# Optimization experiments

Hardware: AMD Instinct MI355X
Metric: run time of the kernel (lower is better)

## Reference

```python
import jax, jax.numpy as jnp
import numpy as np

# dims
B, A, CIN, CC = 512, 256, 7, 16          # batch, num_actions, input channels, conv channels
D, H, DH, E = 48, 8, 6, 512              # token_dimension, heads, head_dim, num_embeddings
S, T = 32, 32                            # num_input_tokens, num_output_tokens
AH = H * DH                              # 48
NL = 4                                   # attention layers
CONV_IN = A * CC                         # 4096
ENC = S * D                              # 1536
DEC_OUT = A * CIN                        # 1792
SCALE = float(np.sqrt(D))                # module uses sqrt(input_embedding_dim)
EPS = 1e-5


def _ln(x, g, b):
    m = jnp.mean(x, axis=-1, keepdims=True)
    v = jnp.var(x, axis=-1, keepdims=True)
    return (x - m) * jax.lax.rsqrt(v + EPS) * g + b


def setup_inputs() -> dict:
    key = jax.random.key(0)
    ks = iter(jax.random.split(key, 64))
    def rn(shape, s=0.05):
        return jax.random.normal(next(ks), shape, dtype=jnp.float32) * s
    inp = {}
    inp['x'] = jax.random.normal(next(ks), (B, A, CIN), dtype=jnp.float32)
    inp['u'] = jax.random.uniform(next(ks), (T, B), dtype=jnp.float32)
    inp['bn_g'] = jnp.ones((CIN,), jnp.float32); inp['bn_b'] = jnp.zeros((CIN,), jnp.float32)
    inp['conv_w'] = rn((CC, CIN, 5)); inp['conv_b'] = jnp.zeros((CC,), jnp.float32)
    inp['tk_W1'] = rn((CONV_IN, 2 * CONV_IN)); inp['tk_b1'] = jnp.zeros((2 * CONV_IN,), jnp.float32)
    inp['tk_W2'] = rn((2 * CONV_IN, ENC)); inp['tk_b2'] = jnp.zeros((ENC,), jnp.float32)
    for nm in ('q', 'k', 'v'):
        inp['ln%s_g' % nm] = jnp.ones((NL, D), jnp.float32)
        inp['ln%s_b' % nm] = jnp.zeros((NL, D), jnp.float32)
        inp['W%s' % nm] = rn((NL, D, AH))
        inp['b%s' % nm] = jnp.zeros((NL, AH), jnp.float32)
    inp['Wo'] = rn((NL, AH, D)); inp['bo'] = jnp.zeros((NL, D), jnp.float32)
    inp['mln_g'] = jnp.ones((NL, D), jnp.float32); inp['mln_b'] = jnp.zeros((NL, D), jnp.float32)
    inp['W1'] = rn((NL, D, 2 * D)); inp['b1'] = jnp.zeros((NL, 2 * D), jnp.float32)
    inp['W2'] = rn((NL, 2 * D, D)); inp['b2'] = jnp.zeros((NL, D), jnp.float32)
    inp['emb'] = rn((D, E), 1.0)          # nn.Parameter(torch.randn(D, E))
    inp['pos_enc'] = rn((T, D), 1.0)      # nn.Parameter(torch.randn(T, D))
    inp['dec_W1'] = rn((ENC, 2 * ENC)); inp['dec_b1'] = jnp.zeros((2 * ENC,), jnp.float32)
    inp['dec_W2'] = rn((2 * ENC, DEC_OUT)); inp['dec_b2'] = jnp.zeros((DEC_OUT,), jnp.float32)
    return inp


def _fwd(x, u, bn_g, bn_b, conv_w, conv_b, tk_W1, tk_b1, tk_W2, tk_b2,
         lnq_g, lnq_b, Wq, bq, lnk_g, lnk_b, Wk, bk, lnv_g, lnv_b, Wv, bv, Wo, bo,
         mln_g, mln_b, W1, b1, W2, b2, emb, pos_enc, dec_W1, dec_b1, dec_W2, dec_b2):
    # --- conv stem (BatchNorm1d in training mode: batch statistics) ---
    xt = x.transpose(0, 2, 1)                              # [B, 7, A]
    mu = jnp.mean(xt, axis=(0, 2), keepdims=True)
    var = jnp.var(xt, axis=(0, 2), keepdims=True)
    xn = (xt - mu) * jax.lax.rsqrt(var + EPS) * bn_g[None, :, None] + bn_b[None, :, None]
    xc = jax.lax.conv_general_dilated(xn, conv_w, (1,), ((2, 2),),
                                      dimension_numbers=('NCH', 'OIH', 'NCH')) + conv_b[None, :, None]
    xf = xc.reshape(B, -1)                                 # [B, 16*A]
    h = jax.nn.relu(xf @ tk_W1 + tk_b1)
    toks = (h @ tk_W2 + tk_b2).reshape(B, S, D)            # [B, S, D]

    STOT = S + T
    kc = jnp.zeros((NL, B, H, STOT, DH), jnp.float32)
    vc = jnp.zeros_like(kc)

    # --- prefill pass (output discarded; fills KV caches) ---
    ii = jnp.arange(S)[:, None]; jj = jnp.arange(S)[None, :]
    pre_mask = jnp.where(jj - ii >= S - 1, -999.0, 0.0)    # triu(-999, diagonal=S-1), as in source
    xcur = toks
    for l in range(NL):
        q = (_ln(xcur, lnq_g[l], lnq_b[l]) @ Wq[l] + bq[l]).reshape(B, S, H, DH).transpose(0, 2, 1, 3)
        k = (_ln(xcur, lnk_g[l], lnk_b[l]) @ Wk[l] + bk[l]).reshape(B, S, H, DH).transpose(0, 2, 1, 3)
        v = (_ln(xcur, lnv_g[l], lnv_b[l]) @ Wv[l] + bv[l]).reshape(B, S, H, DH).transpose(0, 2, 1, 3)
        kc = kc.at[l, :, :, :S].set(k)
        vc = vc.at[l, :, :, :S].set(v)
        attn = jax.nn.softmax(jnp.einsum('bhqd,bhkd->bhqk', q, k) / SCALE + pre_mask, axis=-1)
        o = jnp.einsum('bhqk,bhkd->bhqd', attn, v).transpose(0, 2, 1, 3).reshape(B, S, AH)
        xcur = o @ Wo[l] + bo[l] + xcur
        hh = jax.nn.relu(_ln(xcur, mln_g[l], mln_b[l]) @ W1[l] + b1[l])
        xcur = hh @ W2[l] + b2[l]

    jidx = jnp.arange(STOT)

    def step(carry, xs):
        kc, vc = carry
        i, pe, uu = xs
        p = S + i                                          # cache length before this step
        xtk = jnp.broadcast_to(pe, (B, 1, D))
        newk, newv = [], []
        for l in range(NL):
            q = (_ln(xtk, lnq_g[l], lnq_b[l]) @ Wq[l] + bq[l]).reshape(B, 1, H, DH).transpose(0, 2, 1, 3)
            k = (_ln(xtk, lnk_g[l], lnk_b[l]) @ Wk[l] + bk[l]).reshape(B, 1, H, DH).transpose(0, 2, 1, 3)
            v = (_ln(xtk, lnv_g[l], lnv_b[l]) @ Wv[l] + bv[l]).reshape(B, 1, H, DH).transpose(0, 2, 1, 3)
            kcl = jax.lax.dynamic_update_slice(kc[l], k, (0, 0, p, 0))
            vcl = jax.lax.dynamic_update_slice(vc[l], v, (0, 0, p, 0))
            scores = jnp.einsum('bhqd,bhkd->bhqk', q, kcl) / SCALE
            # source mask: -999 added for positions >= mask_offset (includes the new token itself)
            scores = scores + jnp.where(jidx >= p, -999.0, 0.0)
            attn = jax.nn.softmax(scores, axis=-1)
            o = jnp.einsum('bhqk,bhkd->bhqd', attn, vcl).transpose(0, 2, 1, 3).reshape(B, 1, AH)
            xtk = o @ Wo[l] + bo[l] + xtk
            hh = jax.nn.relu(_ln(xtk, mln_g[l], mln_b[l]) @ W1[l] + b1[l])
            xtk = hh @ W2[l] + b2[l]
            newk.append(kcl); newv.append(vcl)
        attended = xtk                                     # [B, 1, D]
        probs = jax.nn.softmax((attended @ emb).reshape(B, E), axis=1)
        cdf = jnp.cumsum(probs, axis=1)
        idx = jnp.clip(jnp.sum((cdf < uu[:, None]).astype(jnp.int32), axis=1), 0, E - 1)
        sel = emb.T[idx].reshape(B, 1, D)
        st = sel + attended - jax.lax.stop_gradient(attended)  # straight-through
        return (jnp.stack(newk), jnp.stack(newv)), st

    (_, _), outs = jax.lax.scan(step, (kc, vc), (jnp.arange(T), pos_enc, u))
    out_tokens = outs.transpose(1, 0, 2, 3).reshape(B, T * D)
    dh_ = jax.nn.relu(out_tokens @ dec_W1 + dec_b1)
    traj = (dh_ @ dec_W2 + dec_b2).reshape(B, A, CIN)
    return traj


def reference(x, u, bn_g, bn_b, conv_w, conv_b, tk_W1, tk_b1, tk_W2, tk_b2,
              lnq_g, lnq_b, Wq, bq, lnk_g, lnk_b, Wk, bk, lnv_g, lnv_b, Wv, bv, Wo, bo,
              mln_g, mln_b, W1, b1, W2, b2, emb, pos_enc, dec_W1, dec_b1, dec_W2, dec_b2):
    return _fwd(x, u, bn_g, bn_b, conv_w, conv_b, tk_W1, tk_b1, tk_W2, tk_b2,
                lnq_g, lnq_b, Wq, bq, lnk_g, lnk_b, Wk, bk, lnv_g, lnv_b, Wv, bv, Wo, bo,
                mln_g, mln_b, W1, b1, W2, b2, emb, pos_enc, dec_W1, dec_b1, dec_W2, dec_b2)
```

## Files before the change

### kernel.cpp

```cpp
#include <hip/hip_runtime.h>

static const double SCALE_ = 6.928203230275509;

__device__ inline float  fma_t(float a, float b, float c)  { return fmaf(a, b, c); }
__device__ inline double fma_t(double a, double b, double c){ return fma(a, b, c); }

__device__ __attribute__((noinline)) double dotW(const double* a,
                                                 const float* W, int n, int ldw,
                                                 double init) {
  double a0 = init, a1 = 0.0;
#pragma unroll 2
  for (int i = 0; i < n; i += 2) {
    a0 = fma(a[i],     (double)W[i * ldw],       a0);
    a1 = fma(a[i + 1], (double)W[(i + 1) * ldw], a1);
  }
  return a0 + a1;
}

template <int N, typename WP>
__device__ __forceinline__ double dotN(const double* a, WP W, int ldw, double init) {
  double c0 = init, c1 = 0.0, c2 = 0.0, c3 = 0.0;
#pragma unroll
  for (int i = 0; i < N; i += 4) {
    c0 = fma(a[i],     (double)W[i * ldw],       c0);
    c1 = fma(a[i + 1], (double)W[(i + 1) * ldw], c1);
    c2 = fma(a[i + 2], (double)W[(i + 2) * ldw], c2);
    c3 = fma(a[i + 3], (double)W[(i + 3) * ldw], c3);
  }
  return (c0 + c1) + (c2 + c3);
}

__device__ __attribute__((noinline)) double2 ln_stats48(const double* x) {
  double s0 = 0, s1 = 0, q0 = 0, q1 = 0;
#pragma unroll 2
  for (int i = 0; i < 48; i += 2) {
    const double va = x[i], vb = x[i + 1];
    s0 += va; q0 = fma(va, va, q0);
    s1 += vb; q1 = fma(vb, vb, q1);
  }
  const double m = (s0 + s1) / 48.0;
  const double rs = 1.0 / sqrt((q0 + q1) / 48.0 - m * m + 1e-5);
  return make_double2(m, rs);
}

__device__ __attribute__((noinline)) double exp_ni(double x) { return exp(x); }

__global__ __launch_bounds__(256) void bn_partial_kernel(const float* __restrict__ x,
                                                         double* __restrict__ part) {
  __shared__ double sh[256 * 14];
  const int tid = threadIdx.x;
  const int idx = blockIdx.x * 256 + tid;
  const float* p = x + (size_t)idx * 7;
  for (int c = 0; c < 7; ++c) {
    double v = (double)p[c];
    sh[tid * 14 + c] = v;
    sh[tid * 14 + 7 + c] = v * v;
  }
  __syncthreads();
  if (tid < 14) {
    double acc = 0.0;
    for (int t = 0; t < 256; ++t) acc += sh[t * 14 + tid];
    part[blockIdx.x * 14 + tid] = acc;
  }
}

__global__ void bn_final_kernel(const double* __restrict__ part,
                                const float* __restrict__ g, const float* __restrict__ bb,
                                double* __restrict__ stat) {
  const int c = threadIdx.x;
  if (c < 7) {
    double s = 0.0, s2 = 0.0;
    for (int i = 0; i < 512; ++i) { s += part[i * 14 + c]; s2 += part[i * 14 + 7 + c]; }
    const double mean = s / 131072.0;
    const double var = s2 / 131072.0 - mean * mean;
    const double rstd = 1.0 / sqrt(var + 1e-5);
    const double scale = rstd * (double)g[c];
    stat[c] = scale;
    stat[7 + c] = (double)bb[c] - mean * scale;
  }
}

__global__ __launch_bounds__(256) void conv_kernel(const float* __restrict__ x,
                                                   const float* __restrict__ wconv,
                                                   const float* __restrict__ cb,
                                                   const double* __restrict__ stat,
                                                   double* __restrict__ xf) {
  __shared__ double wsh[560 + 14];
  const int tid = threadIdx.x;
  for (int i = tid; i < 560; i += 256) wsh[i] = (double)wconv[i];
  for (int i = tid; i < 14; i += 256) wsh[560 + i] = stat[i];
  __syncthreads();
  const int idx = blockIdx.x * 256 + tid;
  const int a = idx & 255;
  const int o = (idx >> 8) & 15;
  const int b = idx >> 12;
  double acc = (double)cb[o];
  const float* xb = x + (size_t)b * (256 * 7);
  for (int k = 0; k < 5; ++k) {
    const int pos = a + k - 2;
    if (pos < 0 || pos >= 256) continue;
    const float* xp = xb + pos * 7;
    for (int ci = 0; ci < 7; ++ci) {
      const double xn = (double)xp[ci] * wsh[560 + ci] + wsh[567 + ci];
      acc = fma(xn, wsh[(o * 7 + ci) * 5 + k], acc);
    }
  }
  xf[idx] = acc;
}

template <typename T, bool BIAS, bool RELU>
__global__ __launch_bounds__(256) void gemm128_kernel(const T* __restrict__ A,
                                                      const float* __restrict__ Bm,
                                                      const float* __restrict__ bias,
                                                      T* __restrict__ C,
                                                      const int M, const int N, const int K,
                                                      const int kc) {
  __shared__ T As[16][130];
  __shared__ T Bs[16][66];
  const int tid = threadIdx.x;
  const int tx = tid & 15, ty = tid >> 4;
  const int n0 = blockIdx.x * 64, m0 = blockIdx.y * 128;
  const int k0 = blockIdx.z * kc, kend = k0 + kc;
  const int ar = tid >> 1, ac = (tid & 1) * 8;
  const int br = tid >> 4, bc = (tid & 15) * 4;
  const T* Ap = A + (size_t)(m0 + ar) * K;
  const float* Bp = Bm + (size_t)br * N + n0 + bc;
  T acc[8][4] = {};
  for (int k = k0; k < kend; k += 16) {
    T av8[8];
#pragma unroll
    for (int i = 0; i < 8; ++i) av8[i] = Ap[k + ac + i];
    const float4 bw = *(const float4*)(Bp + (size_t)k * N);
#pragma unroll
    for (int i = 0; i < 8; ++i) As[ac + i][ar] = av8[i];
    Bs[br][bc] = (T)bw.x; Bs[br][bc + 1] = (T)bw.y;
    Bs[br][bc + 2] = (T)bw.z; Bs[br][bc + 3] = (T)bw.w;
    __syncthreads();
#pragma unroll
    for (int kk = 0; kk < 16; ++kk) {
      T a[8], b[4];
#pragma unroll
      for (int i = 0; i < 8; ++i) a[i] = As[kk][ty * 8 + i];
#pragma unroll
      for (int j = 0; j < 4; ++j) b[j] = Bs[kk][tx * 4 + j];
#pragma unroll
      for (int i = 0; i < 8; ++i)
#pragma unroll
        for (int j = 0; j < 4; ++j) acc[i][j] = fma_t(a[i], b[j], acc[i][j]);
    }
    __syncthreads();
  }
  T* Cp = C + (size_t)blockIdx.z * M * N;
#pragma unroll
  for (int i = 0; i < 8; ++i) {
    const int row = m0 + ty * 8 + i;
#pragma unroll
    for (int j = 0; j < 4; ++j) {
      const int col = n0 + tx * 4 + j;
      T v = acc[i][j];
      if (BIAS) v += (T)bias[col];
      if (RELU) v = v > (T)0 ? v : (T)0;
      Cp[(size_t)row * N + col] = v;
    }
  }
}

template <typename T, bool BIAS, bool RELU>
__global__ __launch_bounds__(256) void gemm_kernel(const T* __restrict__ A,
                                                   const float* __restrict__ Bm,
                                                   const float* __restrict__ bias,
                                                   T* __restrict__ C,
                                                   const int M, const int N, const int K,
                                                   const int kc) {
  __shared__ T As[16][65];
  __shared__ T Bs[16][65];
  const int tid = threadIdx.x;
  const int tx = tid & 15, ty = tid >> 4;
  const int n0 = blockIdx.x * 64, m0 = blockIdx.y * 64;
  const int k0 = blockIdx.z * kc, kend = k0 + kc;
  const int ar = tid >> 2, ac = (tid & 3) * 4;
  const int br = tid >> 4, bc = (tid & 15) * 4;
  const T* Ap = A + (size_t)(m0 + ar) * K;
  const float* Bp = Bm + (size_t)br * N + n0 + bc;
  T acc[4][4] = {};
  for (int k = k0; k < kend; k += 16) {
    const T a0 = Ap[k + ac], a1 = Ap[k + ac + 1], a2 = Ap[k + ac + 2], a3 = Ap[k + ac + 3];
    const float4 bw = *(const float4*)(Bp + (size_t)k * N);
    As[ac][ar] = a0; As[ac + 1][ar] = a1; As[ac + 2][ar] = a2; As[ac + 3][ar] = a3;
    Bs[br][bc] = (T)bw.x; Bs[br][bc + 1] = (T)bw.y; Bs[br][bc + 2] = (T)bw.z; Bs[br][bc + 3] = (T)bw.w;
    __syncthreads();
#pragma unroll
    for (int kk = 0; kk < 16; ++kk) {
      T av[4], bv2[4];
#pragma unroll
      for (int i = 0; i < 4; ++i) av[i] = As[kk][ty * 4 + i];
#pragma unroll
      for (int j = 0; j < 4; ++j) bv2[j] = Bs[kk][tx * 4 + j];
#pragma unroll
      for (int i = 0; i < 4; ++i)
#pragma unroll
        for (int j = 0; j < 4; ++j) acc[i][j] = fma_t(av[i], bv2[j], acc[i][j]);
    }
    __syncthreads();
  }
  T* Cp = C + (size_t)blockIdx.z * M * N;
#pragma unroll
  for (int i = 0; i < 4; ++i) {
    const int row = m0 + ty * 4 + i;
#pragma unroll
    for (int j = 0; j < 4; ++j) {
      const int col = n0 + tx * 4 + j;
      T v = acc[i][j];
      if (BIAS) v += (T)bias[col];
      if (RELU) v = v > (T)0 ? v : (T)0;
      Cp[(size_t)row * N + col] = v;
    }
  }
}

__global__ __launch_bounds__(256) void reduce2_bias_kernel(const double* __restrict__ part,
                                                           const float* __restrict__ bias,
                                                           double* __restrict__ out,
                                                           const int MN, const int N) {
  const int i = blockIdx.x * 256 + threadIdx.x;
  if (i < MN) out[i] = part[i] + part[MN + i] + (double)bias[i % N];
}

__global__ __launch_bounds__(256) void prefill_kernel(
    const double* __restrict__ toks,
    const float* __restrict__ lnq_g, const float* __restrict__ lnq_b,
    const float* __restrict__ Wq, const float* __restrict__ bq,
    const float* __restrict__ lnk_g, const float* __restrict__ lnk_b,
    const float* __restrict__ Wk, const float* __restrict__ bk,
    const float* __restrict__ lnv_g, const float* __restrict__ lnv_b,
    const float* __restrict__ Wv, const float* __restrict__ bvv,
    const float* __restrict__ Wo, const float* __restrict__ bo,
    const float* __restrict__ mln_g, const float* __restrict__ mln_b,
    const float* __restrict__ W1, const float* __restrict__ b1,
    const float* __restrict__ W2, const float* __restrict__ b2,
    double* __restrict__ kcache, double* __restrict__ vcache) {
  const int b = blockIdx.x, tid = threadIdx.x;
  __shared__ double xcur[1536], abuf[1536], qbuf[1536], kvbuf[3072];
  __shared__ double mean[32], rstd[32];
  double* kb = kvbuf;
  double* vb = kvbuf + 1536;

#pragma unroll 1
  for (int i = tid; i < 1536; i += 256) xcur[i] = toks[(size_t)b * 1536 + i];
  __syncthreads();

#pragma unroll 1
  for (int l = 0; l < 4; ++l) {
    if (tid < 32) {
      double s = 0.0, s2 = 0.0;
#pragma unroll 4
      for (int i = 0; i < 48; ++i) { const double v = xcur[tid * 48 + i]; s += v; s2 += v * v; }
      const double m = s / 48.0;
      mean[tid] = m;
      rstd[tid] = 1.0 / sqrt(s2 / 48.0 - m * m + 1e-5);
    }
    __syncthreads();
    const bool last = (l == 3);

    if (!last) {
#pragma unroll 1
      for (int i = tid; i < 1536; i += 256) {
        const int t = i / 48, d = i % 48;
        abuf[i] = (xcur[i] - mean[t]) * rstd[t] * (double)lnq_g[l * 48 + d] + (double)lnq_b[l * 48 + d];
      }
      __syncthreads();
#pragma unroll 1
      for (int i = tid; i < 1536; i += 256) {
        const int t = i / 48, j = i % 48;
        qbuf[i] = dotW(abuf + t * 48, Wq + l * 2304 + j, 48, 48, (double)bq[l * 48 + j]);
      }
      __syncthreads();
    }
#pragma unroll 1
    for (int i = tid; i < 1536; i += 256) {
      const int t = i / 48, d = i % 48;
      abuf[i] = (xcur[i] - mean[t]) * rstd[t] * (double)lnk_g[l * 48 + d] + (double)lnk_b[l * 48 + d];
    }
    __syncthreads();
#pragma unroll 1
    for (int i = tid; i < 1536; i += 256) {
      const int t = i / 48, j = i % 48;
      kb[i] = dotW(abuf + t * 48, Wk + l * 2304 + j, 48, 48, (double)bk[l * 48 + j]);
    }
    __syncthreads();
#pragma unroll 1
    for (int i = tid; i < 1536; i += 256) {
      const int t = i / 48, d = i % 48;
      abuf[i] = (xcur[i] - mean[t]) * rstd[t] * (double)lnv_g[l * 48 + d] + (double)lnv_b[l * 48 + d];
    }
    __syncthreads();
#pragma unroll 1
    for (int i = tid; i < 1536; i += 256) {
      const int t = i / 48, j = i % 48;
      vb[i] = dotW(abuf + t * 48, Wv + l * 2304 + j, 48, 48, (double)bvv[l * 48 + j]);
    }
    __syncthreads();
#pragma unroll 1
    for (int i = tid; i < 1536; i += 256) {
      const int t = i / 48, j = i % 48;
      const int h = j / 6, d = j % 6;
      const size_t ci = ((((size_t)b * 4 + l) * 8 + h) * 64 + t) * 6 + d;
      kcache[ci] = kb[i];
      vcache[ci] = vb[i];
    }

    if (!last) {
      const int t = tid >> 3, h = tid & 7;
      const double* qp = qbuf + t * 48 + h * 6;
      const double q0 = qp[0], q1 = qp[1], q2 = qp[2], q3 = qp[3], q4 = qp[4], q5 = qp[5];
      double mx = -1e300;
#pragma unroll 4
      for (int j = 0; j < 32; ++j) {
        const double* kp = kb + j * 48 + h * 6;
        double sv = q0 * kp[0];
        sv = fma(q1, kp[1], sv); sv = fma(q2, kp[2], sv); sv = fma(q3, kp[3], sv);
        sv = fma(q4, kp[4], sv); sv = fma(q5, kp[5], sv);
        sv /= SCALE_;
        if (t == 0 && j == 31) sv -= 999.0;
        mx = sv > mx ? sv : mx;
      }
      double den = 0, o0 = 0, o1 = 0, o2 = 0, o3 = 0, o4 = 0, o5 = 0;
#pragma unroll 4
      for (int j = 0; j < 32; ++j) {
        const double* kp = kb + j * 48 + h * 6;
        double sv = q0 * kp[0];
        sv = fma(q1, kp[1], sv); sv = fma(q2, kp[2], sv); sv = fma(q3, kp[3], sv);
        sv = fma(q4, kp[4], sv); sv = fma(q5, kp[5], sv);
        sv /= SCALE_;
        if (t == 0 && j == 31) sv -= 999.0;
        const double e = exp_ni(sv - mx);
        den += e;
        const double* vp = vb + j * 48 + h * 6;
        o0 = fma(e, vp[0], o0); o1 = fma(e, vp[1], o1); o2 = fma(e, vp[2], o2);
        o3 = fma(e, vp[3], o3); o4 = fma(e, vp[4], o4); o5 = fma(e, vp[5], o5);
      }
      abuf[t * 48 + h * 6 + 0] = o0 / den;
      abuf[t * 48 + h * 6 + 1] = o1 / den;
      abuf[t * 48 + h * 6 + 2] = o2 / den;
      abuf[t * 48 + h * 6 + 3] = o3 / den;
      abuf[t * 48 + h * 6 + 4] = o4 / den;
      abuf[t * 48 + h * 6 + 5] = o5 / den;
      __syncthreads();
#pragma unroll 1
      for (int i = tid; i < 1536; i += 256) {
        const int t2 = i / 48, j = i % 48;
        xcur[i] += dotW(abuf + t2 * 48, Wo + l * 2304 + j, 48, 48, (double)bo[l * 48 + j]);
      }
      __syncthreads();
      if (tid < 32) {
        double s = 0.0, s2 = 0.0;
#pragma unroll 4
        for (int i = 0; i < 48; ++i) { const double v = xcur[tid * 48 + i]; s += v; s2 += v * v; }
        const double m = s / 48.0;
        mean[tid] = m;
        rstd[tid] = 1.0 / sqrt(s2 / 48.0 - m * m + 1e-5);
      }
      __syncthreads();
#pragma unroll 1
      for (int i = tid; i < 1536; i += 256) {
        const int t2 = i / 48, d = i % 48;
        qbuf[i] = (xcur[i] - mean[t2]) * rstd[t2] * (double)mln_g[l * 48 + d] + (double)mln_b[l * 48 + d];
      }
      __syncthreads();
#pragma unroll 1
      for (int i = tid; i < 3072; i += 256) {
        const int t2 = i / 96, jj = i % 96;
        const double acc = dotW(qbuf + t2 * 48, W1 + l * 4608 + jj, 48, 96, (double)b1[l * 96 + jj]);
        kvbuf[i] = acc > 0 ? acc : 0;
      }
      __syncthreads();
#pragma unroll 1
      for (int i = tid; i < 1536; i += 256) {
        const int t2 = i / 48, j = i % 48;
        abuf[i] = dotW(kvbuf + t2 * 96, W2 + l * 4608 + j, 96, 48, (double)b2[l * 48 + j]);
      }
      __syncthreads();
#pragma unroll 1
      for (int i = tid; i < 1536; i += 256) xcur[i] = abuf[i];
      __syncthreads();
    }
  }
}

__device__ __attribute__((noinline)) void sample_step(
    double* xtk, double* probs, double* red,
    const float* __restrict__ emb, const float* __restrict__ u,
    float* __restrict__ out_tok, int b, int step, int tid) {
  const double lg1 = dotN<48>(xtk, emb + tid, 512, 0.0);
  const double lg2 = dotN<48>(xtk, emb + 256 + tid, 512, 0.0);
  double mx = lg1 > lg2 ? lg1 : lg2;
#pragma unroll
  for (int off = 1; off < 64; off <<= 1) { const double o2 = __shfl_xor(mx, off); mx = o2 > mx ? o2 : mx; }
  if ((tid & 63) == 0) red[tid >> 6] = mx;
  __syncthreads();
  {
    const double m0 = red[0] > red[1] ? red[0] : red[1];
    const double m1 = red[2] > red[3] ? red[2] : red[3];
    mx = m0 > m1 ? m0 : m1;
  }
  probs[tid] = exp(lg1 - mx);
  probs[tid + 256] = exp(lg2 - mx);
  __syncthreads();
  if (tid < 64) {
    const int lane = tid;
    double loc[8], run = 0;
#pragma unroll
    for (int n2 = 0; n2 < 8; ++n2) { run += probs[lane * 8 + n2]; loc[n2] = run; }
    double incl = run;
#pragma unroll
    for (int off = 1; off < 64; off <<= 1) {
      const double t2 = __shfl_up(incl, off);
      if (lane >= off) incl += t2;
    }
    const double excl = incl - run;
    const double Ssum = __shfl(incl, 63);
    const double uu = (double)u[step * 512 + b];
    int cnt = 0;
#pragma unroll
    for (int n2 = 0; n2 < 8; ++n2) cnt += ((excl + loc[n2]) / Ssum < uu) ? 1 : 0;
#pragma unroll
    for (int off = 1; off < 64; off <<= 1) cnt += __shfl_xor(cnt, off);
    const int idx = cnt > 511 ? 511 : cnt;
    if (lane < 48) {
      const double sel = (double)emb[lane * 512 + idx];
      const double att = xtk[lane];
      out_tok[(size_t)b * 1536 + step * 48 + lane] = (float)((sel + att) - att);
    }
  }
  __syncthreads();
}

__global__ __launch_bounds__(256) void ar_kernel(
    const float* __restrict__ pos_enc, const float* __restrict__ u,
    const float* __restrict__ lnq_g, const float* __restrict__ lnq_b,
    const float* __restrict__ Wq, const float* __restrict__ bq,
    const float* __restrict__ lnk_g, const float* __restrict__ lnk_b,
    const float* __restrict__ Wk, const float* __restrict__ bk,
    const float* __restrict__ lnv_g, const float* __restrict__ lnv_b,
    const float* __restrict__ Wv, const float* __restrict__ bvv,
    const float* __restrict__ Wo, const float* __restrict__ bo,
    const float* __restrict__ mln_g, const float* __restrict__ mln_b,
    const float* __restrict__ W1, const float* __restrict__ b1,
    const float* __restrict__ W2, const float* __restrict__ b2,
    const float* __restrict__ emb,
    double* __restrict__ kcache, double* __restrict__ vcache,
    float* __restrict__ out_tok) {
  const int b = blockIdx.x, tid = threadIdx.x;
  __shared__ double xtk[48], anorm[144], qs[48], os[48], hh[96], probs[512], red[4];
  __shared__ float wsh[9216];

#pragma unroll 1
  for (int step = 0; step < 32; ++step) {
    const int p = 32 + step;
    if (tid < 48) xtk[tid] = (double)pos_enc[step * 48 + tid];
    __syncthreads();

#pragma unroll 1
    for (int l = 0; l < 4; ++l) {
      {
        float4* wsh4 = (float4*)wsh;
#pragma unroll 1
        for (int i = tid; i < 2304; i += 256) {
          const int a = i / 576, off4 = i - a * 576;
          const float* src = a == 0 ? Wq : a == 1 ? Wk : a == 2 ? Wv : Wo;
          wsh4[i] = ((const float4*)(src + l * 2304))[off4];
        }
      }
      {
        const double2 st = ln_stats48(xtk);
        if (tid < 144) {
          const int which = tid / 48, d = tid - which * 48;
          const float* gp = which == 0 ? lnq_g : which == 1 ? lnk_g : lnv_g;
          const float* bp = which == 0 ? lnq_b : which == 1 ? lnk_b : lnv_b;
          anorm[tid] = (xtk[d] - st.x) * st.y * (double)gp[l * 48 + d] + (double)bp[l * 48 + d];
        }
      }
      __syncthreads();
      if (tid < 144) {
        const int which = tid / 48, j = tid - which * 48;
        const float* bbp = which == 0 ? bq : which == 1 ? bk : bvv;
        const double acc = dotN<48>(anorm + which * 48, wsh + which * 2304 + j, 48,
                                    (double)bbp[l * 48 + j]);
        if (which == 0) {
          qs[j] = acc;
        } else {
          const int h = j / 6, d = j - h * 6;
          const size_t ci = ((((size_t)b * 4 + l) * 8 + h) * 64 + p) * 6 + d;
          if (which == 1) kcache[ci] = acc; else vcache[ci] = acc;
        }
      }
      __syncthreads();
      {
        const int h = tid >> 5, r = tid & 31;
        const double* kcb = kcache + ((((size_t)b * 4 + l) * 8 + h) * 64) * 6;
        const double* vcb = vcache + ((((size_t)b * 4 + l) * 8 + h) * 64) * 6;
        const double qv0 = qs[h * 6 + 0], qv1 = qs[h * 6 + 1], qv2 = qs[h * 6 + 2],
                     qv3 = qs[h * 6 + 3], qv4 = qs[h * 6 + 4], qv5 = qs[h * 6 + 5];
        const bool has2 = (r + 32) < p;
        const double* kp1 = kcb + r * 6;
        double sv1 = qv0 * kp1[0];
        sv1 = fma(qv1, kp1[1], sv1); sv1 = fma(qv2, kp1[2], sv1); sv1 = fma(qv3, kp1[3], sv1);
        sv1 = fma(qv4, kp1[4], sv1); sv1 = fma(qv5, kp1[5], sv1);
        sv1 /= SCALE_;
        double sv2 = -1e300;
        if (has2) {
          const double* kp2 = kcb + (r + 32) * 6;
          double t2 = qv0 * kp2[0];
          t2 = fma(qv1, kp2[1], t2); t2 = fma(qv2, kp2[2], t2); t2 = fma(qv3, kp2[3], t2);
          t2 = fma(qv4, kp2[4], t2); t2 = fma(qv5, kp2[5], t2);
          sv2 = t2 / SCALE_;
        }
        double mx = sv1 > sv2 ? sv1 : sv2;
#pragma unroll
        for (int off = 1; off < 32; off <<= 1) { const double o2 = __shfl_xor(mx, off); mx = o2 > mx ? o2 : mx; }
        const double e1 = exp(sv1 - mx);
        const double e2 = has2 ? exp(sv2 - mx) : 0.0;
        double den = e1 + e2;
        const double* vp1 = vcb + r * 6;
        double o[6];
#pragma unroll
        for (int d = 0; d < 6; ++d) o[d] = e1 * vp1[d];
        if (has2) {
          const double* vp2 = vcb + (r + 32) * 6;
#pragma unroll
          for (int d = 0; d < 6; ++d) o[d] = fma(e2, vp2[d], o[d]);
        }
#pragma unroll
        for (int off = 1; off < 32; off <<= 1) {
          den += __shfl_xor(den, off);
#pragma unroll
          for (int d = 0; d < 6; ++d) o[d] += __shfl_xor(o[d], off);
        }
        if (r == 0) {
#pragma unroll
          for (int d = 0; d < 6; ++d) os[h * 6 + d] = o[d] / den;
        }
      }
      __syncthreads();
      if (tid < 48)
        xtk[tid] += dotN<48>(os, wsh + 3 * 2304 + tid, 48, (double)bo[l * 48 + tid]);
      __syncthreads();
      {
        float4* wsh4 = (float4*)wsh;
#pragma unroll 1
        for (int i = tid; i < 2304; i += 256) {
          const int a = i / 1152, off4 = i - a * 1152;
          const float* src = a == 0 ? W1 : W2;
          wsh4[i] = ((const float4*)(src + l * 4608))[off4];
        }
      }
      {
        const double2 st = ln_stats48(xtk);
        if (tid < 48)
          anorm[tid] = (xtk[tid] - st.x) * st.y * (double)mln_g[l * 48 + tid] + (double)mln_b[l * 48 + tid];
      }
      __syncthreads();
      if (tid < 96) {
        const double v = dotN<48>(anorm, wsh + tid, 96, (double)b1[l * 96 + tid]);
        hh[tid] = v > 0 ? v : 0;
      }
      __syncthreads();
      if (tid < 48)
        xtk[tid] = dotN<96>(hh, wsh + 4608 + tid, 48, (double)b2[l * 48 + tid]);
      __syncthreads();
    }

    sample_step(xtk, probs, red, emb, u, out_tok, b, step, tid);
  }
}

extern "C" void kernel_launch(void* const* d_in, const int* in_sizes, int n_in,
                              void* d_out, int out_size, void* d_ws, size_t ws_size,
                              hipStream_t stream) {
  const float* x      = (const float*)d_in[0];
  const float* u      = (const float*)d_in[1];
  const float* bn_g   = (const float*)d_in[2];
  const float* bn_b   = (const float*)d_in[3];
  const float* conv_w = (const float*)d_in[4];
  const float* conv_b = (const float*)d_in[5];
  const float* tk_W1  = (const float*)d_in[6];
  const float* tk_b1  = (const float*)d_in[7];
  const float* tk_W2  = (const float*)d_in[8];
  const float* tk_b2  = (const float*)d_in[9];
  const float* lnq_g  = (const float*)d_in[10];
  const float* lnq_b  = (const float*)d_in[11];
  const float* Wq     = (const float*)d_in[12];
  const float* bq     = (const float*)d_in[13];
  const float* lnk_g  = (const float*)d_in[14];
  const float* lnk_b  = (const float*)d_in[15];
  const float* Wk     = (const float*)d_in[16];
  const float* bk     = (const float*)d_in[17];
  const float* lnv_g  = (const float*)d_in[18];
  const float* lnv_b  = (const float*)d_in[19];
  const float* Wv     = (const float*)d_in[20];
  const float* bvv    = (const float*)d_in[21];
  const float* Wo     = (const float*)d_in[22];
  const float* bo     = (const float*)d_in[23];
  const float* mln_g  = (const float*)d_in[24];
  const float* mln_b  = (const float*)d_in[25];
  const float* W1     = (const float*)d_in[26];
  const float* b1     = (const float*)d_in[27];
  const float* W2     = (const float*)d_in[28];
  const float* b2     = (const float*)d_in[29];
  const float* emb    = (const float*)d_in[30];
  const float* pos    = (const float*)d_in[31];
  const float* dW1    = (const float*)d_in[32];
  const float* db1    = (const float*)d_in[33];
  const float* dW2    = (const float*)d_in[34];
  const float* db2    = (const float*)d_in[35];
  float* out = (float*)d_out;

  char* w = (char*)d_ws;
  size_t off = 0;
  auto alloc = [&](size_t bytes) {
    size_t o = off;
    off = (off + bytes + 255) & ~(size_t)255;
    return o;
  };
  const size_t o_bnp  = alloc(512 * 14 * 8);
  const size_t o_bns  = alloc(14 * 8);
  const size_t o_xf   = alloc(16777216);
  const size_t o_h    = alloc(33554432);
  const size_t o_toks = alloc(6291456);
  const size_t o_kc   = alloc(50331648);
  const size_t o_vc   = alloc(50331648);

  double* bnp  = (double*)(w + o_bnp);
  double* bns  = (double*)(w + o_bns);
  double* xf   = (double*)(w + o_xf);
  double* hbuf = (double*)(w + o_h);
  double* toks = (double*)(w + o_toks);
  double* kc   = (double*)(w + o_kc);
  double* vc   = (double*)(w + o_vc);
  double* part = (double*)(w + o_xf);
  float*  otok = (float*)(w + o_h);
  float*  dh   = (float*)(w + o_h + 4194304);

  bn_partial_kernel<<<512, 256, 0, stream>>>(x, bnp);
  bn_final_kernel<<<1, 64, 0, stream>>>(bnp, bn_g, bn_b, bns);
  conv_kernel<<<8192, 256, 0, stream>>>(x, conv_w, conv_b, bns, xf);
  gemm128_kernel<double, true, true><<<dim3(128, 4, 1), 256, 0, stream>>>(
      xf, tk_W1, tk_b1, hbuf, 512, 8192, 4096, 4096);
  gemm128_kernel<double, false, false><<<dim3(24, 4, 2), 256, 0, stream>>>(
      hbuf, tk_W2, nullptr, part, 512, 1536, 8192, 4096);
  reduce2_bias_kernel<<<3072, 256, 0, stream>>>(part, tk_b2, toks, 512 * 1536, 1536);
  prefill_kernel<<<512, 256, 0, stream>>>(toks,
      lnq_g, lnq_b, Wq, bq, lnk_g, lnk_b, Wk, bk, lnv_g, lnv_b, Wv, bvv,
      Wo, bo, mln_g, mln_b, W1, b1, W2, b2, kc, vc);
  ar_kernel<<<512, 256, 0, stream>>>(pos, u,
      lnq_g, lnq_b, Wq, bq, lnk_g, lnk_b, Wk, bk, lnv_g, lnv_b, Wv, bvv,
      Wo, bo, mln_g, mln_b, W1, b1, W2, b2, emb, kc, vc, otok);
  gemm_kernel<float, true, true><<<dim3(48, 8, 1), 256, 0, stream>>>(
      otok, dW1, db1, dh, 512, 3072, 1536, 1536);
  gemm_kernel<float, true, false><<<dim3(28, 8, 1), 256, 0, stream>>>(
      dh, dW2, db2, out, 512, 1792, 3072, 3072);
}
```

Measured before the change: 4.955 ms.

## Widen autoregressive kernel to 512 threads with split-K dot products and warp LN

```diff
diff --git a/kernel.cpp b/kernel.cpp
--- a/kernel.cpp
+++ b/kernel.cpp
@@ -4,18 +4,6 @@
 
 __device__ inline float  fma_t(float a, float b, float c)  { return fmaf(a, b, c); }
 __device__ inline double fma_t(double a, double b, double c){ return fma(a, b, c); }
-
-__device__ __attribute__((noinline)) double dotW(const double* a,
-                                                 const float* W, int n, int ldw,
-                                                 double init) {
-  double a0 = init, a1 = 0.0;
-#pragma unroll 2
-  for (int i = 0; i < n; i += 2) {
-    a0 = fma(a[i],     (double)W[i * ldw],       a0);
-    a1 = fma(a[i + 1], (double)W[(i + 1) * ldw], a1);
-  }
-  return a0 + a1;
-}
 
 template <int N, typename WP>
 __device__ __forceinline__ double dotN(const double* a, WP W, int ldw, double init) {
@@ -28,19 +16,6 @@
     c3 = fma(a[i + 3], (double)W[(i + 3) * ldw], c3);
   }
   return (c0 + c1) + (c2 + c3);
-}
-
-__device__ __attribute__((noinline)) double2 ln_stats48(const double* x) {
-  double s0 = 0, s1 = 0, q0 = 0, q1 = 0;
-#pragma unroll 2
-  for (int i = 0; i < 48; i += 2) {
-    const double va = x[i], vb = x[i + 1];
-    s0 += va; q0 = fma(va, va, q0);
-    s1 += vb; q1 = fma(vb, vb, q1);
-  }
-  const double m = (s0 + s1) / 48.0;
-  const double rs = 1.0 / sqrt((q0 + q1) / 48.0 - m * m + 1e-5);
-  return make_double2(m, rs);
 }
 
 __device__ __attribute__((noinline)) double exp_ni(double x) { return exp(x); }
@@ -272,7 +247,7 @@
 #pragma unroll 1
       for (int i = tid; i < 1536; i += 256) {
         const int t = i / 48, j = i % 48;
-        qbuf[i] = dotW(abuf + t * 48, Wq + l * 2304 + j, 48, 48, (double)bq[l * 48 + j]);
+        qbuf[i] = dotN<48>(abuf + t * 48, Wq + l * 2304 + j, 48, (double)bq[l * 48 + j]);
       }
       __syncthreads();
     }
@@ -285,7 +260,7 @@
 #pragma unroll 1
     for (int i = tid; i < 1536; i += 256) {
       const int t = i / 48, j = i % 48;
-      kb[i] = dotW(abuf + t * 48, Wk + l * 2304 + j, 48, 48, (double)bk[l * 48 + j]);
+      kb[i] = dotN<48>(abuf + t * 48, Wk + l * 2304 + j, 48, (double)bk[l * 48 + j]);
     }
     __syncthreads();
 #pragma unroll 1
@@ -297,7 +272,7 @@
 #pragma unroll 1
     for (int i = tid; i < 1536; i += 256) {
       const int t = i / 48, j = i % 48;
-      vb[i] = dotW(abuf + t * 48, Wv + l * 2304 + j, 48, 48, (double)bvv[l * 48 + j]);
+      vb[i] = dotN<48>(abuf + t * 48, Wv + l * 2304 + j, 48, (double)bvv[l * 48 + j]);
     }
     __syncthreads();
 #pragma unroll 1
@@ -349,7 +324,7 @@
 #pragma unroll 1
       for (int i = tid; i < 1536; i += 256) {
         const int t2 = i / 48, j = i % 48;
-        xcur[i] += dotW(abuf + t2 * 48, Wo + l * 2304 + j, 48, 48, (double)bo[l * 48 + j]);
+        xcur[i] += dotN<48>(abuf + t2 * 48, Wo + l * 2304 + j, 48, (double)bo[l * 48 + j]);
       }
       __syncthreads();
       if (tid < 32) {
@@ -370,14 +345,14 @@
 #pragma unroll 1
       for (int i = tid; i < 3072; i += 256) {
         const int t2 = i / 96, jj = i % 96;
-        const double acc = dotW(qbuf + t2 * 48, W1 + l * 4608 + jj, 48, 96, (double)b1[l * 96 + jj]);
+        const double acc = dotN<48>(qbuf + t2 * 48, W1 + l * 4608 + jj, 96, (double)b1[l * 96 + jj]);
         kvbuf[i] = acc > 0 ? acc : 0;
       }
       __syncthreads();
 #pragma unroll 1
       for (int i = tid; i < 1536; i += 256) {
         const int t2 = i / 48, j = i % 48;
-        abuf[i] = dotW(kvbuf + t2 * 96, W2 + l * 4608 + j, 96, 48, (double)b2[l * 48 + j]);
+        abuf[i] = dotN<96>(kvbuf + t2 * 96, W2 + l * 4608 + j, 48, (double)b2[l * 48 + j]);
       }
       __syncthreads();
 #pragma unroll 1
@@ -391,20 +366,18 @@
     double* xtk, double* probs, double* red,
     const float* __restrict__ emb, const float* __restrict__ u,
     float* __restrict__ out_tok, int b, int step, int tid) {
-  const double lg1 = dotN<48>(xtk, emb + tid, 512, 0.0);
-  const double lg2 = dotN<48>(xtk, emb + 256 + tid, 512, 0.0);
-  double mx = lg1 > lg2 ? lg1 : lg2;
-#pragma unroll
-  for (int off = 1; off < 64; off <<= 1) { const double o2 = __shfl_xor(mx, off); mx = o2 > mx ? o2 : mx; }
-  if ((tid & 63) == 0) red[tid >> 6] = mx;
-  __syncthreads();
   {
-    const double m0 = red[0] > red[1] ? red[0] : red[1];
-    const double m1 = red[2] > red[3] ? red[2] : red[3];
-    mx = m0 > m1 ? m0 : m1;
-  }
-  probs[tid] = exp(lg1 - mx);
-  probs[tid + 256] = exp(lg2 - mx);
+    const double lg = dotN<48>(xtk, emb + tid, 512, 0.0);
+    double mx = lg;
+#pragma unroll
+    for (int off = 1; off < 64; off <<= 1) { const double o2 = __shfl_xor(mx, off); mx = o2 > mx ? o2 : mx; }
+    if ((tid & 63) == 0) red[tid >> 6] = mx;
+    __syncthreads();
+    mx = red[0];
+#pragma unroll
+    for (int wv = 1; wv < 8; ++wv) mx = red[wv] > mx ? red[wv] : mx;
+    probs[tid] = exp_ni(lg - mx);
+  }
   __syncthreads();
   if (tid < 64) {
     const int lane = tid;
@@ -435,7 +408,7 @@
   __syncthreads();
 }
 
-__global__ __launch_bounds__(256) void ar_kernel(
+__global__ __launch_bounds__(512) void ar_kernel(
     const float* __restrict__ pos_enc, const float* __restrict__ u,
     const float* __restrict__ lnq_g, const float* __restrict__ lnq_b,
     const float* __restrict__ Wq, const float* __restrict__ bq,
@@ -451,7 +424,7 @@
     double* __restrict__ kcache, double* __restrict__ vcache,
     float* __restrict__ out_tok) {
   const int b = blockIdx.x, tid = threadIdx.x;
-  __shared__ double xtk[48], anorm[144], qs[48], os[48], hh[96], probs[512], red[4];
+  __shared__ double xtk[48], anorm[144], qs[48], os[48], hh[96], probs[512], red[8];
   __shared__ float wsh[9216];
 
 #pragma unroll 1
@@ -462,76 +435,80 @@
 
 #pragma unroll 1
     for (int l = 0; l < 4; ++l) {
-      {
+      if (tid < 64) {
+        const double v = tid < 48 ? xtk[tid] : 0.0;
+        double s = v, s2 = v * v;
+#pragma unroll
+        for (int off = 32; off; off >>= 1) { s += __shfl_xor(s, off); s2 += __shfl_xor(s2, off); }
+        const double m = s / 48.0;
+        const double rs = 1.0 / sqrt(s2 / 48.0 - m * m + 1e-5);
+        if (tid < 48) {
+          const double xn = (xtk[tid] - m) * rs;
+          anorm[tid]       = xn * (double)lnq_g[l * 48 + tid] + (double)lnq_b[l * 48 + tid];
+          anorm[48 + tid]  = xn * (double)lnk_g[l * 48 + tid] + (double)lnk_b[l * 48 + tid];
+          anorm[96 + tid]  = xn * (double)lnv_g[l * 48 + tid] + (double)lnv_b[l * 48 + tid];
+        }
+      } else {
         float4* wsh4 = (float4*)wsh;
 #pragma unroll 1
-        for (int i = tid; i < 2304; i += 256) {
+        for (int i = tid - 64; i < 2304; i += 448) {
           const int a = i / 576, off4 = i - a * 576;
           const float* src = a == 0 ? Wq : a == 1 ? Wk : a == 2 ? Wv : Wo;
           wsh4[i] = ((const float4*)(src + l * 2304))[off4];
         }
       }
+      __syncthreads();
+      if (tid < 288) {
+        const int o = tid >> 1, half = tid & 1;
+        const int which = o / 48, j = o - which * 48;
+        const float* bbp = which == 0 ? bq : which == 1 ? bk : bvv;
+        const double init = half == 0 ? (double)bbp[l * 48 + j] : 0.0;
+        const double* an = anorm + which * 48 + half * 24;
+        const float* wp = wsh + which * 2304 + half * 1152 + j;
+        double a0 = init, a1 = 0.0;
+#pragma unroll
+        for (int i = 0; i < 24; i += 2) {
+          a0 = fma(an[i],     (double)wp[i * 48],       a0);
+          a1 = fma(an[i + 1], (double)wp[(i + 1) * 48], a1);
+        }
+        const double mine = a0 + a1;
+        const double tot = mine + __shfl_xor(mine, 1);
+        if (half == 0) {
+          if (which == 0) {
+            qs[j] = tot;
+          } else {
+            const int h = j / 6, d = j - h * 6;
+            const size_t ci = ((((size_t)b * 4 + l) * 8 + h) * 64 + p) * 6 + d;
+            if (which == 1) kcache[ci] = tot; else vcache[ci] = tot;
+          }
+        }
+      }
+      __syncthreads();
       {
-        const double2 st = ln_stats48(xtk);
-        if (tid < 144) {
-          const int which = tid / 48, d = tid - which * 48;
-          const float* gp = which == 0 ? lnq_g : which == 1 ? lnk_g : lnv_g;
-          const float* bp = which == 0 ? lnq_b : which == 1 ? lnk_b : lnv_b;
-          anorm[tid] = (xtk[d] - st.x) * st.y * (double)gp[l * 48 + d] + (double)bp[l * 48 + d];
-        }
-      }
-      __syncthreads();
-      if (tid < 144) {
-        const int which = tid / 48, j = tid - which * 48;
-        const float* bbp = which == 0 ? bq : which == 1 ? bk : bvv;
-        const double acc = dotN<48>(anorm + which * 48, wsh + which * 2304 + j, 48,
-                                    (double)bbp[l * 48 + j]);
-        if (which == 0) {
-          qs[j] = acc;
-        } else {
-          const int h = j / 6, d = j - h * 6;
-          const size_t ci = ((((size_t)b * 4 + l) * 8 + h) * 64 + p) * 6 + d;
-          if (which == 1) kcache[ci] = acc; else vcache[ci] = acc;
-        }
-      }
-      __syncthreads();
-      {
-        const int h = tid >> 5, r = tid & 31;
+        const int h = tid >> 6, r = tid & 63;
+        const bool act = r < p;
+        const int rr = act ? r : 0;
         const double* kcb = kcache + ((((size_t)b * 4 + l) * 8 + h) * 64) * 6;
         const double* vcb = vcache + ((((size_t)b * 4 + l) * 8 + h) * 64) * 6;
         const double qv0 = qs[h * 6 + 0], qv1 = qs[h * 6 + 1], qv2 = qs[h * 6 + 2],
                      qv3 = qs[h * 6 + 3], qv4 = qs[h * 6 + 4], qv5 = qs[h * 6 + 5];
-        const bool has2 = (r + 32) < p;
-        const double* kp1 = kcb + r * 6;
-        double sv1 = qv0 * kp1[0];
-        sv1 = fma(qv1, kp1[1], sv1); sv1 = fma(qv2, kp1[2], sv1); sv1 = fma(qv3, kp1[3], sv1);
-        sv1 = fma(qv4, kp1[4], sv1); sv1 = fma(qv5, kp1[5], sv1);
-        sv1 /= SCALE_;
-        double sv2 = -1e300;
-        if (has2) {
-          const double* kp2 = kcb + (r + 32) * 6;
-          double t2 = qv0 * kp2[0];
-          t2 = fma(qv1, kp2[1], t2); t2 = fma(qv2, kp2[2], t2); t2 = fma(qv3, kp2[3], t2);
-          t2 = fma(qv4, kp2[4], t2); t2 = fma(qv5, kp2[5], t2);
-          sv2 = t2 / SCALE_;
-        }
-        double mx = sv1 > sv2 ? sv1 : sv2;
-#pragma unroll
-        for (int off = 1; off < 32; off <<= 1) { const double o2 = __shfl_xor(mx, off); mx = o2 > mx ? o2 : mx; }
-        const double e1 = exp(sv1 - mx);
-        const double e2 = has2 ? exp(sv2 - mx) : 0.0;
-        double den = e1 + e2;
-        const double* vp1 = vcb + r * 6;
+        const double* kp = kcb + rr * 6;
+        double sv = qv0 * kp[0];
+        sv = fma(qv1, kp[1], sv); sv = fma(qv2, kp[2], sv); sv = fma(qv3, kp[3], sv);
+        sv = fma(qv4, kp[4], sv); sv = fma(qv5, kp[5], sv);
+        sv /= SCALE_;
+        if (!act) sv = -1e300;
+        double mx = sv;
+#pragma unroll
+        for (int off = 1; off < 64; off <<= 1) { const double o2 = __shfl_xor(mx, off); mx = o2 > mx ? o2 : mx; }
+        const double e = act ? exp(sv - mx) : 0.0;
+        const double* vp = vcb + rr * 6;
+        double den = e;
         double o[6];
 #pragma unroll
-        for (int d = 0; d < 6; ++d) o[d] = e1 * vp1[d];
-        if (has2) {
-          const double* vp2 = vcb + (r + 32) * 6;
-#pragma unroll
-          for (int d = 0; d < 6; ++d) o[d] = fma(e2, vp2[d], o[d]);
-        }
-#pragma unroll
-        for (int off = 1; off < 32; off <<= 1) {
+        for (int d = 0; d < 6; ++d) o[d] = e * vp[d];
+#pragma unroll
+        for (int off = 1; off < 64; off <<= 1) {
           den += __shfl_xor(den, off);
 #pragma unroll
           for (int d = 0; d < 6; ++d) o[d] += __shfl_xor(o[d], off);
@@ -542,31 +519,61 @@
         }
       }
       __syncthreads();
-      if (tid < 48)
-        xtk[tid] += dotN<48>(os, wsh + 3 * 2304 + tid, 48, (double)bo[l * 48 + tid]);
-      __syncthreads();
-      {
+      if (tid < 192) {
+        const int o = tid >> 2, q = tid & 3;
+        double s = q == 0 ? (double)bo[l * 48 + o] : 0.0;
+        const double* a = os + q * 12;
+        const float* wp = wsh + 3 * 2304 + q * 576 + o;
+#pragma unroll
+        for (int i = 0; i < 12; ++i) s = fma(a[i], (double)wp[i * 48], s);
+        s += __shfl_xor(s, 1);
+        s += __shfl_xor(s, 2);
+        if (q == 0) xtk[o] += s;
+      }
+      __syncthreads();
+      if (tid < 64) {
+        const double v = tid < 48 ? xtk[tid] : 0.0;
+        double s = v, s2 = v * v;
+#pragma unroll
+        for (int off = 32; off; off >>= 1) { s += __shfl_xor(s, off); s2 += __shfl_xor(s2, off); }
+        const double m = s / 48.0;
+        const double rs = 1.0 / sqrt(s2 / 48.0 - m * m + 1e-5);
+        if (tid < 48)
+          anorm[tid] = (xtk[tid] - m) * rs * (double)mln_g[l * 48 + tid] + (double)mln_b[l * 48 + tid];
+      } else {
         float4* wsh4 = (float4*)wsh;
 #pragma unroll 1
-        for (int i = tid; i < 2304; i += 256) {
+        for (int i = tid - 64; i < 2304; i += 448) {
           const int a = i / 1152, off4 = i - a * 1152;
           const float* src = a == 0 ? W1 : W2;
           wsh4[i] = ((const float4*)(src + l * 4608))[off4];
         }
       }
-      {
-        const double2 st = ln_stats48(xtk);
-        if (tid < 48)
-          anorm[tid] = (xtk[tid] - st.x) * st.y * (double)mln_g[l * 48 + tid] + (double)mln_b[l * 48 + tid];
-      }
-      __syncthreads();
-      if (tid < 96) {
-        const double v = dotN<48>(anorm, wsh + tid, 96, (double)b1[l * 96 + tid]);
-        hh[tid] = v > 0 ? v : 0;
-      }
-      __syncthreads();
-      if (tid < 48)
-        xtk[tid] = dotN<96>(hh, wsh + 4608 + tid, 48, (double)b2[l * 48 + tid]);
+      __syncthreads();
+      if (tid < 384) {
+        const int o = tid >> 2, q = tid & 3;
+        double s = q == 0 ? (double)b1[l * 96 + o] : 0.0;
+        const double* a = anorm + q * 12;
+        const float* wp = wsh + q * 1152 + o;
+#pragma unroll
+        for (int i = 0; i < 12; ++i) s = fma(a[i], (double)wp[i * 96], s);
+        s += __shfl_xor(s, 1);
+        s += __shfl_xor(s, 2);
+        if (q == 0) hh[o] = s > 0 ? s : 0;
+      }
+      __syncthreads();
+      if (tid < 384) {
+        const int o = tid >> 3, q = tid & 7;
+        double s = q == 0 ? (double)b2[l * 48 + o] : 0.0;
+        const double* a = hh + q * 12;
+        const float* wp = wsh + 4608 + q * 576 + o;
+#pragma unroll
+        for (int i = 0; i < 12; ++i) s = fma(a[i], (double)wp[i * 48], s);
+        s += __shfl_xor(s, 1);
+        s += __shfl_xor(s, 2);
+        s += __shfl_xor(s, 4);
+        if (q == 0) xtk[o] = s;
+      }
       __syncthreads();
     }
 
@@ -646,13 +653,13 @@
   conv_kernel<<<8192, 256, 0, stream>>>(x, conv_w, conv_b, bns, xf);
   gemm128_kernel<double, true, true><<<dim3(128, 4, 1), 256, 0, stream>>>(
       xf, tk_W1, tk_b1, hbuf, 512, 8192, 4096, 4096);
-  gemm128_kernel<double, false, false><<<dim3(24, 4, 2), 256, 0, stream>>>(
+  gemm_kernel<double, false, false><<<dim3(24, 8, 2), 256, 0, stream>>>(
       hbuf, tk_W2, nullptr, part, 512, 1536, 8192, 4096);
   reduce2_bias_kernel<<<3072, 256, 0, stream>>>(part, tk_b2, toks, 512 * 1536, 1536);
   prefill_kernel<<<512, 256, 0, stream>>>(toks,
       lnq_g, lnq_b, Wq, bq, lnk_g, lnk_b, Wk, bk, lnv_g, lnv_b, Wv, bvv,
       Wo, bo, mln_g, mln_b, W1, b1, W2, b2, kc, vc);
-  ar_kernel<<<512, 256, 0, stream>>>(pos, u,
+  ar_kernel<<<512, 512, 0, stream>>>(pos, u,
       lnq_g, lnq_b, Wq, bq, lnk_g, lnk_b, Wk, bk, lnv_g, lnv_b, Wv, bvv,
       Wo, bo, mln_g, mln_b, W1, b1, W2, b2, emb, kc, vc, otok);
   gemm_kernel<float, true, true><<<dim3(48, 8, 1), 256, 0, stream>>>(
```

After: 5.618 ms. +13.4%, slower.
